# Performance work log

Measured on AMD Instinct MI355X. Metric: run time of the kernel, lower is better.

## Reference

```python
import jax, jax.numpy as jnp
import numpy as np

K_HOPS = 3  # spektral TAGConv default
BN_EPS = 1e-3  # keras BatchNormalization default epsilon


def _propagate(x, edge_src, edge_dst, edge_weight, n_nodes):
    # y[dst] += w * x[src]  (sparse adjacency @ x)
    msg = x[edge_src] * edge_weight[:, None]
    return jax.ops.segment_sum(msg, edge_dst, num_segments=n_nodes)


def _tag_conv(x, edge_src, edge_dst, edge_weight, W, b):
    n = x.shape[0]
    hops = [x]
    h = x
    for _ in range(K_HOPS):
        h = _propagate(h, edge_src, edge_dst, edge_weight, n)
        hops.append(h)
    # concat hops along features then dense combine: [N, F*(K+1)] @ [F*(K+1), C]
    return jnp.concatenate(hops, axis=-1) @ W + b


def setup_inputs() -> dict:
    key = jax.random.key(0)
    ks = jax.random.split(key, 6)
    N, F, E, H, L = 20000, 2000, 640000, 128, 15
    x = jax.random.normal(ks[0], (N, F), dtype=jnp.float32)
    edge_src = jax.random.randint(ks[1], (E,), 0, N, dtype=jnp.int32)
    edge_dst = jax.random.randint(ks[2], (E,), 0, N, dtype=jnp.int32)
    # normalized adjacency weights, roughly 1/avg_degree scale
    edge_weight = jax.random.uniform(ks[3], (E,), dtype=jnp.float32) / 32.0
    W1 = jax.random.normal(ks[4], (F * (K_HOPS + 1), H), dtype=jnp.float32) * (1.0 / np.sqrt(F * (K_HOPS + 1)))
    b1 = jnp.zeros((H,), dtype=jnp.float32)
    gamma = jnp.ones((H,), dtype=jnp.float32)
    beta = jnp.zeros((H,), dtype=jnp.float32)
    moving_mean = jnp.zeros((H,), dtype=jnp.float32)
    moving_var = jnp.ones((H,), dtype=jnp.float32)
    W2 = jax.random.normal(ks[5], (H * (K_HOPS + 1), L), dtype=jnp.float32) * (1.0 / np.sqrt(H * (K_HOPS + 1)))
    b2 = jnp.zeros((L,), dtype=jnp.float32)
    return {"x": x, "edge_src": edge_src, "edge_dst": edge_dst, "edge_weight": edge_weight,
            "W1": W1, "b1": b1, "gamma": gamma, "beta": beta,
            "moving_mean": moving_mean, "moving_var": moving_var, "W2": W2, "b2": b2}


def reference(x, edge_src, edge_dst, edge_weight, W1, b1, gamma, beta,
              moving_mean, moving_var, W2, b2):
    # training=False: Dropout is identity, BN uses moving statistics
    h = _tag_conv(x, edge_src, edge_dst, edge_weight, W1, b1)
    h = (h - moving_mean) * jax.lax.rsqrt(moving_var + BN_EPS) * gamma + beta
    h = jax.nn.relu(h)
    z = _tag_conv(h, edge_src, edge_dst, edge_weight, W2, b2)
    return z
```

## Files before the change

kernel.cpp:

```cpp
#include <hip/hip_runtime.h>
#include <hip/hip_bf16.h>
#include <cstdint>
#include <cstddef>

#define N_NODES 20000
#define F_IN    2000
#define H_DIM   128
#define L_DIM   15
#define K_PAD   2048
#define YS      384
#define BM      128
#define BN      64
#define BK      32
#define I_TILES 157

#define FSW(r) (((r) + ((r) >> 2)) & 3)

typedef __attribute__((ext_vector_type(4))) float f32x4;
typedef __attribute__((ext_vector_type(8))) short s16x8;
typedef __attribute__((ext_vector_type(8))) unsigned short u16x8;

__device__ __forceinline__ unsigned short f2bf(float f) {
  unsigned int u = __float_as_uint(f);
  u += 0x7fff + ((u >> 16) & 1);
  return (unsigned short)(u >> 16);
}

__device__ __forceinline__ unsigned int pkbf(float a, float b) {
  union { __hip_bfloat162 h; unsigned int u; } cv;
  cv.h = __float22bfloat162_rn(make_float2(a, b));
  return cv.u;
}

__device__ __forceinline__ float2 bf2f(unsigned int u) {
  float2 r;
  r.x = __uint_as_float(u << 16);
  r.y = __uint_as_float(u & 0xffff0000u);
  return r;
}

__global__ __launch_bounds__(256) void k_cvt_x(const float* __restrict__ x,
                                               unsigned short* __restrict__ xb) {
  unsigned int t = blockIdx.x * 256u + threadIdx.x;
  unsigned int row = t >> 8;
  unsigned int colB = (t & 255u) * 8u;
  u16x8 o = {0, 0, 0, 0, 0, 0, 0, 0};
  if (colB < F_IN) {
    const float4 a = *(const float4*)(x + (size_t)row * F_IN + colB);
    const float4 b = *(const float4*)(x + (size_t)row * F_IN + colB + 4);
    o[0] = f2bf(a.x); o[1] = f2bf(a.y); o[2] = f2bf(a.z); o[3] = f2bf(a.w);
    o[4] = f2bf(b.x); o[5] = f2bf(b.y); o[6] = f2bf(b.z); o[7] = f2bf(b.w);
  }
  unsigned int s  = (colB >> 3) & 3;
  unsigned int sp = s ^ FSW(row & 15);
  *(u16x8*)(xb + (size_t)row * K_PAD + (colB & ~31u) + sp * 8) = o;
}

__global__ __launch_bounds__(256) void k_cvt_w1(const float* __restrict__ W1,
                                                unsigned short* __restrict__ bt) {
  __shared__ unsigned short tile[128 * 67];
  const int hop = blockIdx.x >> 5;
  const int k0  = (blockIdx.x & 31) * 64;
  const int t = threadIdx.x;
#pragma unroll
  for (int it = 0; it < 8; ++it) {
    int f4 = it * 256 + t;
    int r  = f4 >> 5;
    int c4 = f4 & 31;
    int k = k0 + r;
    float4 v = make_float4(0.f, 0.f, 0.f, 0.f);
    if (k < F_IN) v = *(const float4*)(W1 + (size_t)(hop * F_IN + k) * H_DIM + c4 * 4);
    tile[(c4 * 4 + 0) * 67 + r] = f2bf(v.x);
    tile[(c4 * 4 + 1) * 67 + r] = f2bf(v.y);
    tile[(c4 * 4 + 2) * 67 + r] = f2bf(v.z);
    tile[(c4 * 4 + 3) * 67 + r] = f2bf(v.w);
  }
  __syncthreads();
  const int c = t >> 1, kh = (t & 1) * 32;
  const int fN = FSW(c & 15);
  unsigned short* dst = bt + (size_t)(hop * 128 + c) * K_PAD + k0 + kh;
  const unsigned short* srcp = tile + c * 67 + kh;
#pragma unroll
  for (int q = 0; q < 4; ++q) {
    u16x8 o;
#pragma unroll
    for (int e = 0; e < 8; ++e) o[e] = srcp[q * 8 + e];
    *(u16x8*)(dst + (q ^ fN) * 8) = o;
  }
}

__global__ __launch_bounds__(256) void k_gemm1(const unsigned short* __restrict__ A,
                                               const unsigned short* __restrict__ B,
                                               float* __restrict__ Y,
                                               unsigned short* __restrict__ Yb3) {
  __shared__ unsigned short As[BM * BK];
  __shared__ unsigned short Bs[BN * BK];
  const int b = blockIdx.x;
  const int i_tile = (b & 7) + 8 * (b >> 6);
  const int j_tile = (b >> 3) & 7;
  if (i_tile >= I_TILES) return;
  const int rowA0 = i_tile * BM;
  const int colB0 = j_tile * BN;
  const int tid  = threadIdx.x;
  const int lane = tid & 63;
  const int wave = tid >> 6;
  const int wm = (wave >> 1) * 64;
  const int wn = (wave & 1) * 32;
  const int quad = lane >> 4;
  const int l15  = lane & 15;
  const int qs   = (quad ^ FSW(l15)) * 8;
  f32x4 acc[4][2] = {};

  for (int kt = 0; kt < K_PAD; kt += BK) {
#pragma unroll
    for (int r = 0; r < 2; ++r) {
      int c = r * 256 + tid;
      int row = c >> 2;
      int kc = (c & 3) * 8;
      const unsigned short* ga = A + (size_t)(rowA0 + row) * K_PAD + kt + kc;
      __builtin_amdgcn_global_load_lds((const __attribute__((address_space(1))) void*)ga,
                                       (__attribute__((address_space(3))) void*)(As + c * 8),
                                       16, 0, 0);
    }
    {
      int c = tid;
      int row = c >> 2;
      int kc = (c & 3) * 8;
      const unsigned short* gb = B + (size_t)(colB0 + row) * K_PAD + kt + kc;
      __builtin_amdgcn_global_load_lds((const __attribute__((address_space(1))) void*)gb,
                                       (__attribute__((address_space(3))) void*)(Bs + c * 8),
                                       16, 0, 0);
    }
    __syncthreads();
    s16x8 af[4], bfr[2];
#pragma unroll
    for (int i = 0; i < 4; ++i)
      af[i] = *(const s16x8*)(As + (wm + i * 16 + l15) * BK + qs);
#pragma unroll
    for (int j = 0; j < 2; ++j)
      bfr[j] = *(const s16x8*)(Bs + (wn + j * 16 + l15) * BK + qs);
#pragma unroll
    for (int i = 0; i < 4; ++i)
#pragma unroll
      for (int j = 0; j < 2; ++j)
        acc[i][j] = __builtin_amdgcn_mfma_f32_16x16x32_bf16(af[i], bfr[j], acc[i][j], 0, 0, 0);
    __syncthreads();
  }

#pragma unroll
  for (int i = 0; i < 4; ++i) {
    int row0 = rowA0 + wm + i * 16 + quad * 4;
#pragma unroll
    for (int j = 0; j < 2; ++j) {
      int gcol = colB0 + wn + j * 16 + l15;
#pragma unroll
      for (int r = 0; r < 4; ++r) {
        int row = row0 + r;
        if (row < N_NODES) {
          if (j_tile < 6)
            Y[(size_t)row * YS + gcol] = acc[i][j][r];
          else
            Yb3[(size_t)row * H_DIM + (gcol - 384)] = f2bf(acc[i][j][r]);
        }
      }
    }
  }
}

__global__ __launch_bounds__(256) void k_hist(const int* __restrict__ dst,
                                              int* __restrict__ deg, int E) {
  int i = blockIdx.x * 256 + threadIdx.x;
  int e = i * 4;
  if (e + 4 <= E) {
    int4 d4 = *(const int4*)(dst + e);
    atomicAdd(&deg[d4.x], 1); atomicAdd(&deg[d4.y], 1);
    atomicAdd(&deg[d4.z], 1); atomicAdd(&deg[d4.w], 1);
  } else {
    for (; e < E; ++e) atomicAdd(&deg[dst[e]], 1);
  }
}

__global__ __launch_bounds__(1024) void k_scan(const int* __restrict__ deg,
                                               int* __restrict__ rowStart,
                                               int* __restrict__ cursor,
                                               int* __restrict__ realEnd) {
  __shared__ int sums[1024];
  const int t = threadIdx.x;
  const int chunk = (N_NODES + 1023) / 1024;
  int lo = t * chunk;
  int hi = lo + chunk; if (hi > N_NODES) hi = N_NODES;
  int s = 0;
  for (int i = lo; i < hi; ++i) s += (deg[i] + 15) & ~15;
  sums[t] = s;
  __syncthreads();
  for (int off = 1; off < 1024; off <<= 1) {
    int v = sums[t];
    int u = (t >= off) ? sums[t - off] : 0;
    __syncthreads();
    sums[t] = v + u;
    __syncthreads();
  }
  int run = sums[t] - s;
  for (int i = lo; i < hi; ++i) {
    rowStart[i] = run; cursor[i] = run; realEnd[i] = run + deg[i];
    run += (deg[i] + 15) & ~15;
  }
  if (t == 1023) rowStart[N_NODES] = run;
}

__global__ __launch_bounds__(256) void k_scatter(const int* __restrict__ src,
                                                 const int* __restrict__ dst,
                                                 const float* __restrict__ w,
                                                 int* cursor,
                                                 int2* __restrict__ eSW, int E) {
  int e = blockIdx.x * 256 + threadIdx.x;
  if (e >= E) return;
  int p = atomicAdd(&cursor[dst[e]], 1);
  eSW[p] = make_int2(src[e], __float_as_int(w[e]));
}

__global__ __launch_bounds__(256) void k_pad(const int* __restrict__ rowStart,
                                             const int* __restrict__ realEnd,
                                             int2* __restrict__ eSW) {
  int t = blockIdx.x * 256 + threadIdx.x;
  int d = t >> 4, i = t & 15;
  if (d >= N_NODES) return;
  int s = realEnd[d] + i;
  if (s < rowStart[d + 1]) eSW[s] = make_int2(0, 0);
}

__global__ __launch_bounds__(256) void k_prop128f(const int* __restrict__ rowStart,
    const int2* __restrict__ eSW,
    const unsigned short* __restrict__ gsrc,
    const float* __restrict__ addv, int addStride, int addOff,
    unsigned short* __restrict__ outb, float* __restrict__ outf,
    const float* __restrict__ b1, const float* __restrict__ gamma,
    const float* __restrict__ beta, const float* __restrict__ mean,
    const float* __restrict__ var, int doBN) {
  const int lane = threadIdx.x & 63;
  const int wave = threadIdx.x >> 6;
  const int eidx = lane >> 4;
  const int s16  = lane & 15;
  const int d = blockIdx.x * 4 + wave;
  const int s0 = rowStart[d], s1 = rowStart[d + 1];
  f32x4 a0 = {0.f, 0.f, 0.f, 0.f};
  f32x4 a1 = {0.f, 0.f, 0.f, 0.f};

  const int nc = (s1 - s0) >> 4;
  int j = s0;
  int2 ed0[4], ed1[4];
  if (nc > 0) {
#pragma unroll
    for (int i = 0; i < 4; ++i) ed0[i] = eSW[j + 4 * i + eidx];
  }
  for (int c = 0; c < nc; ++c) {
    uint4 g[4];
#pragma unroll
    for (int i = 0; i < 4; ++i)
      g[i] = *(const uint4*)(gsrc + (size_t)ed0[i].x * H_DIM + s16 * 8);
    if (c + 1 < nc) {
#pragma unroll
      for (int i = 0; i < 4; ++i) ed1[i] = eSW[j + 16 + 4 * i + eidx];
    }
#pragma unroll
    for (int i = 0; i < 4; ++i) {
      float w = __int_as_float(ed0[i].y);
      float2 p0 = bf2f(g[i].x), p1 = bf2f(g[i].y);
      float2 p2 = bf2f(g[i].z), p3 = bf2f(g[i].w);
      a0.x = fmaf(w, p0.x, a0.x); a0.y = fmaf(w, p0.y, a0.y);
      a0.z = fmaf(w, p1.x, a0.z); a0.w = fmaf(w, p1.y, a0.w);
      a1.x = fmaf(w, p2.x, a1.x); a1.y = fmaf(w, p2.y, a1.y);
      a1.z = fmaf(w, p3.x, a1.z); a1.w = fmaf(w, p3.y, a1.w);
    }
#pragma unroll
    for (int i = 0; i < 4; ++i) ed0[i] = ed1[i];
    j += 16;
  }
  a0.x += __shfl_xor(a0.x, 16); a0.y += __shfl_xor(a0.y, 16);
  a0.z += __shfl_xor(a0.z, 16); a0.w += __shfl_xor(a0.w, 16);
  a1.x += __shfl_xor(a1.x, 16); a1.y += __shfl_xor(a1.y, 16);
  a1.z += __shfl_xor(a1.z, 16); a1.w += __shfl_xor(a1.w, 16);
  a0.x += __shfl_xor(a0.x, 32); a0.y += __shfl_xor(a0.y, 32);
  a0.z += __shfl_xor(a0.z, 32); a0.w += __shfl_xor(a0.w, 32);
  a1.x += __shfl_xor(a1.x, 32); a1.y += __shfl_xor(a1.y, 32);
  a1.z += __shfl_xor(a1.z, 32); a1.w += __shfl_xor(a1.w, 32);
  if (lane >= 16) return;
  const int c8 = s16 * 8;
  const float* ap = addv + (size_t)d * addStride + addOff + c8;
  float4 av0 = *(const float4*)ap;
  float4 av1 = *(const float4*)(ap + 4);
  float r0 = av0.x + a0.x, r1 = av0.y + a0.y, r2 = av0.z + a0.z, r3 = av0.w + a0.w;
  float r4 = av1.x + a1.x, r5 = av1.y + a1.y, r6 = av1.z + a1.z, r7 = av1.w + a1.w;
  if (doBN) {
    float4 bb0 = *(const float4*)(b1 + c8),    bb1 = *(const float4*)(b1 + c8 + 4);
    float4 gg0 = *(const float4*)(gamma + c8), gg1 = *(const float4*)(gamma + c8 + 4);
    float4 be0 = *(const float4*)(beta + c8),  be1 = *(const float4*)(beta + c8 + 4);
    float4 mm0 = *(const float4*)(mean + c8),  mm1 = *(const float4*)(mean + c8 + 4);
    float4 vv0 = *(const float4*)(var + c8),   vv1 = *(const float4*)(var + c8 + 4);
    r0 = (r0 + bb0.x - mm0.x) * rsqrtf(vv0.x + 1e-3f) * gg0.x + be0.x;
    r1 = (r1 + bb0.y - mm0.y) * rsqrtf(vv0.y + 1e-3f) * gg0.y + be0.y;
    r2 = (r2 + bb0.z - mm0.z) * rsqrtf(vv0.z + 1e-3f) * gg0.z + be0.z;
    r3 = (r3 + bb0.w - mm0.w) * rsqrtf(vv0.w + 1e-3f) * gg0.w + be0.w;
    r4 = (r4 + bb1.x - mm1.x) * rsqrtf(vv1.x + 1e-3f) * gg1.x + be1.x;
    r5 = (r5 + bb1.y - mm1.y) * rsqrtf(vv1.y + 1e-3f) * gg1.y + be1.y;
    r6 = (r6 + bb1.z - mm1.z) * rsqrtf(vv1.z + 1e-3f) * gg1.z + be1.z;
    r7 = (r7 + bb1.w - mm1.w) * rsqrtf(vv1.w + 1e-3f) * gg1.w + be1.w;
    r0 = r0 > 0.f ? r0 : 0.f; r1 = r1 > 0.f ? r1 : 0.f;
    r2 = r2 > 0.f ? r2 : 0.f; r3 = r3 > 0.f ? r3 : 0.f;
    r4 = r4 > 0.f ? r4 : 0.f; r5 = r5 > 0.f ? r5 : 0.f;
    r6 = r6 > 0.f ? r6 : 0.f; r7 = r7 > 0.f ? r7 : 0.f;
    float* op = outf + (size_t)d * H_DIM + c8;
    *(float4*)op = make_float4(r0, r1, r2, r3);
    *(float4*)(op + 4) = make_float4(r4, r5, r6, r7);
  } else {
    *(uint4*)(outb + (size_t)d * H_DIM + c8) =
        make_uint4(pkbf(r0, r1), pkbf(r2, r3), pkbf(r4, r5), pkbf(r6, r7));
  }
}

__global__ __launch_bounds__(256) void k_gemm2(const float* __restrict__ Hh,
                                               const float* __restrict__ W2,
                                               float* __restrict__ Y2) {
  __shared__ float w2s[512 * 15];
  for (int i = threadIdx.x; i < 512 * 15; i += 256) w2s[i] = W2[i];
  __syncthreads();
  const int c = threadIdx.x & 63;
  const int d = blockIdx.x * 4 + (threadIdx.x >> 6);
  if (c >= 60 || d >= N_NODES) return;
  const int hop = c / 15, j = c % 15;
  const float4* hr4 = (const float4*)(Hh + (size_t)d * H_DIM);
  float acc = 0.f;
#pragma unroll 8
  for (int k4 = 0; k4 < 32; ++k4) {
    float4 h = hr4[k4];
    const float* wp = w2s + ((hop << 7) + k4 * 4) * 15 + j;
    acc = fmaf(h.x, wp[0],  acc);
    acc = fmaf(h.y, wp[15], acc);
    acc = fmaf(h.z, wp[30], acc);
    acc = fmaf(h.w, wp[45], acc);
  }
  Y2[(size_t)d * 64 + hop * 16 + j] = acc;
}

__global__ __launch_bounds__(256) void k_prop15g(const int* __restrict__ rowStart,
    const int2* __restrict__ eSW,
    const float* __restrict__ in, int inStride, int inOff,
    const float* __restrict__ addv, int addStride, int addOff,
    const float* __restrict__ bias, float* __restrict__ out, int outStride) {
  const int lane = threadIdx.x & 63;
  const int wave = threadIdx.x >> 6;
  const int eidx = lane >> 2, fc = lane & 3;
  const int d = blockIdx.x * 4 + wave;
  const int s0 = rowStart[d], s1 = rowStart[d + 1];
  float4 acc = make_float4(0.f, 0.f, 0.f, 0.f);
  const int nc = (s1 - s0) >> 4;
  int j = s0;
  int2 ed = make_int2(0, 0);
  if (nc > 0) ed = eSW[j + eidx];
  for (int c = 0; c < nc; ++c) {
    float4 g = *(const float4*)(in + (size_t)ed.x * inStride + inOff + fc * 4);
    int2 edn = ed;
    if (c + 1 < nc) edn = eSW[j + 16 + eidx];
    float w = __int_as_float(ed.y);
    acc.x = fmaf(w, g.x, acc.x); acc.y = fmaf(w, g.y, acc.y);
    acc.z = fmaf(w, g.z, acc.z); acc.w = fmaf(w, g.w, acc.w);
    ed = edn; j += 16;
  }
#pragma unroll
  for (int m = 4; m <= 32; m <<= 1) {
    acc.x += __shfl_xor(acc.x, m); acc.y += __shfl_xor(acc.y, m);
    acc.z += __shfl_xor(acc.z, m); acc.w += __shfl_xor(acc.w, m);
  }
  if (lane >= 4) return;
  float4 av = *(const float4*)(addv + (size_t)d * addStride + addOff + fc * 4);
  float r0 = av.x + acc.x, r1 = av.y + acc.y, r2 = av.z + acc.z, r3 = av.w + acc.w;
  if (outStride == 16) {
    *(float4*)(out + (size_t)d * 16 + fc * 4) = make_float4(r0, r1, r2, r3);
  } else {
    float* op = out + (size_t)d * 15 + fc * 4;
    if (fc < 3) {
      float4 bb = *(const float4*)(bias + fc * 4);
      *(float4*)op = make_float4(r0 + bb.x, r1 + bb.y, r2 + bb.z, r3 + bb.w);
    } else {
      op[0] = r0 + bias[12];
      op[1] = r1 + bias[13];
      op[2] = r2 + bias[14];
    }
  }
}

extern "C" void kernel_launch(void* const* d_in, const int* in_sizes, int n_in,
                              void* d_out, int out_size, void* d_ws, size_t ws_size,
                              hipStream_t stream) {
  const float* x     = (const float*)d_in[0];
  const int*   esrc  = (const int*)d_in[1];
  const int*   edst  = (const int*)d_in[2];
  const float* ew    = (const float*)d_in[3];
  const float* W1    = (const float*)d_in[4];
  const float* b1    = (const float*)d_in[5];
  const float* gamma = (const float*)d_in[6];
  const float* beta  = (const float*)d_in[7];
  const float* mmean = (const float*)d_in[8];
  const float* mvar  = (const float*)d_in[9];
  const float* W2    = (const float*)d_in[10];
  const float* b2    = (const float*)d_in[11];
  const int E = in_sizes[1];
  char* ws = (char*)d_ws;

  unsigned short* xb  = (unsigned short*)(ws);
  float*          Y   = (float*)(ws + 81920000);
  unsigned short* Yb3 = (unsigned short*)(ws + 112640000);
  unsigned short* w1r = (unsigned short*)(ws + 117760000);
  int2*           eSW = (int2*)(ws + 119857152);
  int*       deg      = (int*)(ws + 127537152);
  int*       rowStart = (int*)(ws + 127617280);
  int*       cursor   = (int*)(ws + 127697408);
  int*       realEnd  = (int*)(ws + 127777536);
  unsigned short* P   = (unsigned short*)(ws);
  unsigned short* Q   = (unsigned short*)(ws + 5120000);
  float*          Hb  = (float*)(ws + 10240000);
  float*          Y2  = (float*)(ws + 20480000);
  float*          zP  = (float*)(ws + 25600000);
  float*          zQ  = (float*)(ws + 26880000);
  float*          zout = (float*)d_out;

  hipMemsetAsync(deg, 0, N_NODES * sizeof(int), stream);

  k_hist<<<(E / 4 + 255) / 256 + 1, 256, 0, stream>>>(edst, deg, E);
  k_scan<<<1, 1024, 0, stream>>>(deg, rowStart, cursor, realEnd);
  k_scatter<<<(E + 255) / 256, 256, 0, stream>>>(esrc, edst, ew, cursor, eSW, E);
  k_pad<<<(N_NODES * 16) / 256, 256, 0, stream>>>(rowStart, realEnd, eSW);

  k_cvt_x<<<(N_NODES * K_PAD / 8) / 256, 256, 0, stream>>>(x, xb);
  k_cvt_w1<<<128, 256, 0, stream>>>(W1, w1r);
  k_gemm1<<<1280, 256, 0, stream>>>(xb, w1r, Y, Yb3);

  k_prop128f<<<N_NODES / 4, 256, 0, stream>>>(rowStart, eSW, Yb3, Y, YS, 256,
                                              P, nullptr, b1, gamma, beta, mmean, mvar, 0);
  k_prop128f<<<N_NODES / 4, 256, 0, stream>>>(rowStart, eSW, P, Y, YS, 128,
                                              Q, nullptr, b1, gamma, beta, mmean, mvar, 0);
  k_prop128f<<<N_NODES / 4, 256, 0, stream>>>(rowStart, eSW, Q, Y, YS, 0,
                                              nullptr, Hb, b1, gamma, beta, mmean, mvar, 1);

  k_gemm2<<<N_NODES / 4, 256, 0, stream>>>(Hb, W2, Y2);
  k_prop15g<<<N_NODES / 4, 256, 0, stream>>>(rowStart, eSW, Y2, 64, 48, Y2, 64, 32, nullptr, zP, 16);
  k_prop15g<<<N_NODES / 4, 256, 0, stream>>>(rowStart, eSW, zP, 16, 0, Y2, 64, 16, nullptr, zQ, 16);
  k_prop15g<<<N_NODES / 4, 256, 0, stream>>>(rowStart, eSW, zQ, 16, 0, Y2, 64, 0, b2, zout, 15);
}
```

Before: 583.8 us.

## Double GEMM k-step per barrier, parallelize CSR scan, pad rows to 8

The GEMM now loads two BK=32 slabs into separate LDS buffers and runs both before each barrier pair, halving the synchronization count per K. The single-block serial scan over degrees becomes a three-kernel multi-block scan (block sums, scan of block sums, fill). CSR row padding drops from 16 to 8, with a tail path in both propagation kernels for a leftover group of 8 edges, cutting wasted padded-edge work. This adds two kernel launches and slightly more LDS per GEMM block.

```diff
diff --git a/kernel.cpp b/kernel.cpp
--- a/kernel.cpp
+++ b/kernel.cpp
@@ -93,8 +93,8 @@
                                                const unsigned short* __restrict__ B,
                                                float* __restrict__ Y,
                                                unsigned short* __restrict__ Yb3) {
-  __shared__ unsigned short As[BM * BK];
-  __shared__ unsigned short Bs[BN * BK];
+  __shared__ unsigned short As[2][BM * BK];
+  __shared__ unsigned short Bs[2][BN * BK];
   const int b = blockIdx.x;
   const int i_tile = (b & 7) + 8 * (b >> 6);
   const int j_tile = (b >> 3) & 7;
@@ -111,39 +111,45 @@
   const int qs   = (quad ^ FSW(l15)) * 8;
   f32x4 acc[4][2] = {};
 
-  for (int kt = 0; kt < K_PAD; kt += BK) {
-#pragma unroll
-    for (int r = 0; r < 2; ++r) {
-      int c = r * 256 + tid;
-      int row = c >> 2;
-      int kc = (c & 3) * 8;
-      const unsigned short* ga = A + (size_t)(rowA0 + row) * K_PAD + kt + kc;
-      __builtin_amdgcn_global_load_lds((const __attribute__((address_space(1))) void*)ga,
-                                       (__attribute__((address_space(3))) void*)(As + c * 8),
-                                       16, 0, 0);
-    }
-    {
-      int c = tid;
-      int row = c >> 2;
-      int kc = (c & 3) * 8;
-      const unsigned short* gb = B + (size_t)(colB0 + row) * K_PAD + kt + kc;
-      __builtin_amdgcn_global_load_lds((const __attribute__((address_space(1))) void*)gb,
-                                       (__attribute__((address_space(3))) void*)(Bs + c * 8),
-                                       16, 0, 0);
-    }
-    __syncthreads();
-    s16x8 af[4], bfr[2];
-#pragma unroll
-    for (int i = 0; i < 4; ++i)
-      af[i] = *(const s16x8*)(As + (wm + i * 16 + l15) * BK + qs);
-#pragma unroll
-    for (int j = 0; j < 2; ++j)
-      bfr[j] = *(const s16x8*)(Bs + (wn + j * 16 + l15) * BK + qs);
-#pragma unroll
-    for (int i = 0; i < 4; ++i)
+  for (int kt = 0; kt < K_PAD; kt += 64) {
+#pragma unroll
+    for (int h = 0; h < 2; ++h) {
+#pragma unroll
+      for (int r = 0; r < 2; ++r) {
+        int c = r * 256 + tid;
+        int row = c >> 2;
+        int kc = (c & 3) * 8;
+        const unsigned short* ga = A + (size_t)(rowA0 + row) * K_PAD + kt + h * 32 + kc;
+        __builtin_amdgcn_global_load_lds((const __attribute__((address_space(1))) void*)ga,
+                                         (__attribute__((address_space(3))) void*)(As[h] + c * 8),
+                                         16, 0, 0);
+      }
+      {
+        int c = tid;
+        int row = c >> 2;
+        int kc = (c & 3) * 8;
+        const unsigned short* gb = B + (size_t)(colB0 + row) * K_PAD + kt + h * 32 + kc;
+        __builtin_amdgcn_global_load_lds((const __attribute__((address_space(1))) void*)gb,
+                                         (__attribute__((address_space(3))) void*)(Bs[h] + c * 8),
+                                         16, 0, 0);
+      }
+    }
+    __syncthreads();
+#pragma unroll
+    for (int h = 0; h < 2; ++h) {
+      s16x8 af[4], bfr[2];
+#pragma unroll
+      for (int i = 0; i < 4; ++i)
+        af[i] = *(const s16x8*)(As[h] + (wm + i * 16 + l15) * BK + qs);
 #pragma unroll
       for (int j = 0; j < 2; ++j)
-        acc[i][j] = __builtin_amdgcn_mfma_f32_16x16x32_bf16(af[i], bfr[j], acc[i][j], 0, 0, 0);
+        bfr[j] = *(const s16x8*)(Bs[h] + (wn + j * 16 + l15) * BK + qs);
+#pragma unroll
+      for (int i = 0; i < 4; ++i)
+#pragma unroll
+        for (int j = 0; j < 2; ++j)
+          acc[i][j] = __builtin_amdgcn_mfma_f32_16x16x32_bf16(af[i], bfr[j], acc[i][j], 0, 0, 0);
+    }
     __syncthreads();
   }
 
@@ -180,32 +186,62 @@
   }
 }
 
-__global__ __launch_bounds__(1024) void k_scan(const int* __restrict__ deg,
-                                               int* __restrict__ rowStart,
-                                               int* __restrict__ cursor,
-                                               int* __restrict__ realEnd) {
-  __shared__ int sums[1024];
-  const int t = threadIdx.x;
-  const int chunk = (N_NODES + 1023) / 1024;
-  int lo = t * chunk;
-  int hi = lo + chunk; if (hi > N_NODES) hi = N_NODES;
-  int s = 0;
-  for (int i = lo; i < hi; ++i) s += (deg[i] + 15) & ~15;
-  sums[t] = s;
+__global__ __launch_bounds__(256) void k_bsum(const int* __restrict__ deg,
+                                              int* __restrict__ bsum) {
+  __shared__ int red[256];
+  int g = blockIdx.x * 256 + threadIdx.x;
+  int pd = 0;
+  if (g < N_NODES) pd = (deg[g] + 7) & ~7;
+  red[threadIdx.x] = pd;
   __syncthreads();
-  for (int off = 1; off < 1024; off <<= 1) {
-    int v = sums[t];
-    int u = (t >= off) ? sums[t - off] : 0;
-    __syncthreads();
-    sums[t] = v + u;
-    __syncthreads();
-  }
-  int run = sums[t] - s;
-  for (int i = lo; i < hi; ++i) {
-    rowStart[i] = run; cursor[i] = run; realEnd[i] = run + deg[i];
-    run += (deg[i] + 15) & ~15;
-  }
-  if (t == 1023) rowStart[N_NODES] = run;
+  for (int o = 128; o > 0; o >>= 1) {
+    if (threadIdx.x < (unsigned)o) red[threadIdx.x] += red[threadIdx.x + o];
+    __syncthreads();
+  }
+  if (threadIdx.x == 0) bsum[blockIdx.x] = red[0];
+}
+
+__global__ __launch_bounds__(128) void k_scan80(const int* __restrict__ bsum,
+                                                int* __restrict__ boff) {
+  __shared__ int s[128];
+  int t = threadIdx.x;
+  int v = (t < 79) ? bsum[t] : 0;
+  s[t] = v;
+  __syncthreads();
+  for (int o = 1; o < 128; o <<= 1) {
+    int cur = s[t];
+    int u = (t >= o) ? s[t - o] : 0;
+    __syncthreads();
+    s[t] = cur + u;
+    __syncthreads();
+  }
+  if (t < 79) boff[t] = s[t] - v;
+}
+
+__global__ __launch_bounds__(256) void k_fill(const int* __restrict__ deg,
+                                              const int* __restrict__ boff,
+                                              int* __restrict__ rowStart,
+                                              int* __restrict__ cursor,
+                                              int* __restrict__ realEnd) {
+  __shared__ int s[256];
+  int t = threadIdx.x;
+  int g = blockIdx.x * 256 + t;
+  int dv = (g < N_NODES) ? deg[g] : 0;
+  int pd = (dv + 7) & ~7;
+  s[t] = pd;
+  __syncthreads();
+  for (int o = 1; o < 256; o <<= 1) {
+    int cur = s[t];
+    int u = (t >= o) ? s[t - o] : 0;
+    __syncthreads();
+    s[t] = cur + u;
+    __syncthreads();
+  }
+  int rs = boff[blockIdx.x] + s[t] - pd;
+  if (g < N_NODES) {
+    rowStart[g] = rs; cursor[g] = rs; realEnd[g] = rs + dv;
+    if (g == N_NODES - 1) rowStart[N_NODES] = rs + pd;
+  }
 }
 
 __global__ __launch_bounds__(256) void k_scatter(const int* __restrict__ src,
@@ -223,7 +259,7 @@
                                              const int* __restrict__ realEnd,
                                              int2* __restrict__ eSW) {
   int t = blockIdx.x * 256 + threadIdx.x;
-  int d = t >> 4, i = t & 15;
+  int d = t >> 3, i = t & 7;
   if (d >= N_NODES) return;
   int s = realEnd[d] + i;
   if (s < rowStart[d + 1]) eSW[s] = make_int2(0, 0);
@@ -246,7 +282,8 @@
   f32x4 a0 = {0.f, 0.f, 0.f, 0.f};
   f32x4 a1 = {0.f, 0.f, 0.f, 0.f};
 
-  const int nc = (s1 - s0) >> 4;
+  const int n = s1 - s0;
+  const int nc = n >> 4;
   int j = s0;
   int2 ed0[4], ed1[4];
   if (nc > 0) {
@@ -275,6 +312,22 @@
 #pragma unroll
     for (int i = 0; i < 4; ++i) ed0[i] = ed1[i];
     j += 16;
+  }
+  if (n & 8) {
+    int2 ta[2];
+    ta[0] = eSW[j + eidx];
+    ta[1] = eSW[j + 4 + eidx];
+#pragma unroll
+    for (int i = 0; i < 2; ++i) {
+      uint4 g = *(const uint4*)(gsrc + (size_t)ta[i].x * H_DIM + s16 * 8);
+      float w = __int_as_float(ta[i].y);
+      float2 p0 = bf2f(g.x), p1 = bf2f(g.y);
+      float2 p2 = bf2f(g.z), p3 = bf2f(g.w);
+      a0.x = fmaf(w, p0.x, a0.x); a0.y = fmaf(w, p0.y, a0.y);
+      a0.z = fmaf(w, p1.x, a0.z); a0.w = fmaf(w, p1.y, a0.w);
+      a1.x = fmaf(w, p2.x, a1.x); a1.y = fmaf(w, p2.y, a1.y);
+      a1.z = fmaf(w, p3.x, a1.z); a1.w = fmaf(w, p3.y, a1.w);
+    }
   }
   a0.x += __shfl_xor(a0.x, 16); a0.y += __shfl_xor(a0.y, 16);
   a0.z += __shfl_xor(a0.z, 16); a0.w += __shfl_xor(a0.w, 16);
@@ -353,7 +406,8 @@
   const int d = blockIdx.x * 4 + wave;
   const int s0 = rowStart[d], s1 = rowStart[d + 1];
   float4 acc = make_float4(0.f, 0.f, 0.f, 0.f);
-  const int nc = (s1 - s0) >> 4;
+  const int n = s1 - s0;
+  const int nc = n >> 4;
   int j = s0;
   int2 ed = make_int2(0, 0);
   if (nc > 0) ed = eSW[j + eidx];
@@ -365,6 +419,13 @@
     acc.x = fmaf(w, g.x, acc.x); acc.y = fmaf(w, g.y, acc.y);
     acc.z = fmaf(w, g.z, acc.z); acc.w = fmaf(w, g.w, acc.w);
     ed = edn; j += 16;
+  }
+  if ((n & 8) && eidx < 8) {
+    int2 e = eSW[j + eidx];
+    float4 g = *(const float4*)(in + (size_t)e.x * inStride + inOff + fc * 4);
+    float w = __int_as_float(e.y);
+    acc.x = fmaf(w, g.x, acc.x); acc.y = fmaf(w, g.y, acc.y);
+    acc.z = fmaf(w, g.z, acc.z); acc.w = fmaf(w, g.w, acc.w);
   }
 #pragma unroll
   for (int m = 4; m <= 32; m <<= 1) {
@@ -416,6 +477,8 @@
   int*       rowStart = (int*)(ws + 127617280);
   int*       cursor   = (int*)(ws + 127697408);
   int*       realEnd  = (int*)(ws + 127777536);
+  int*       bsum     = (int*)(ws + 127857664);
+  int*       boff     = (int*)(ws + 127858176);
   unsigned short* P   = (unsigned short*)(ws);
   unsigned short* Q   = (unsigned short*)(ws + 5120000);
   float*          Hb  = (float*)(ws + 10240000);
@@ -427,9 +490,11 @@
   hipMemsetAsync(deg, 0, N_NODES * sizeof(int), stream);
 
   k_hist<<<(E / 4 + 255) / 256 + 1, 256, 0, stream>>>(edst, deg, E);
-  k_scan<<<1, 1024, 0, stream>>>(deg, rowStart, cursor, realEnd);
+  k_bsum<<<79, 256, 0, stream>>>(deg, bsum);
+  k_scan80<<<1, 128, 0, stream>>>(bsum, boff);
+  k_fill<<<79, 256, 0, stream>>>(deg, boff, rowStart, cursor, realEnd);
   k_scatter<<<(E + 255) / 256, 256, 0, stream>>>(esrc, edst, ew, cursor, eSW, E);
-  k_pad<<<(N_NODES * 16) / 256, 256, 0, stream>>>(rowStart, realEnd, eSW);
+  k_pad<<<(N_NODES * 8) / 256, 256, 0, stream>>>(rowStart, realEnd, eSW);
 
   k_cvt_x<<<(N_NODES * K_PAD / 8) / 256, 256, 0, stream>>>(x, xb);
   k_cvt_w1<<<128, 256, 0, stream>>>(W1, w1r);
```

Result: faster. 527.3 us (-9.7%).
